# Performance work log

Hardware: AMD Instinct MI355X
Metric: run time of the kernel (lower is better)

## Reference

```python
import jax, jax.numpy as jnp
import numpy as np


def _gauss_kernel(scale):
    # se3cnn.util low_pass_filter: sigma = 0.5*sqrt(scale^2-1), size ~ 1+2*2.5*sigma (odd)
    sigma = 0.5 * float(np.sqrt(scale ** 2 - 1))
    size = int(1 + 2 * 2.5 * sigma)
    if size % 2 == 0:
        size += 1
    r = np.arange(size, dtype=np.float64) - size // 2
    g = np.exp(-r ** 2 / (2 * sigma ** 2))
    k3 = g[:, None, None] * g[None, :, None] * g[None, None, :]
    return (k3 / k3.sum()).astype(np.float32)

_K2 = jnp.asarray(_gauss_kernel(2))  # 5x5x5 Gaussian, scale=2
_DN = ('NCDHW', 'OIDHW', 'NCDHW')


def low_pass(x, stride):
    # depthwise Gaussian blur, padding = size//2 (=2)
    C = x.shape[1]
    k = jnp.tile(_K2[None, None], (C, 1, 1, 1, 1))  # [C,1,5,5,5]
    return jax.lax.conv_general_dilated(x, k, (stride,) * 3, [(2, 2)] * 3,
                                         dimension_numbers=_DN, feature_group_count=C)


def conv3d(x, w, pad):
    return jax.lax.conv_general_dilated(x, w, (1, 1, 1), [(pad, pad)] * 3,
                                         dimension_numbers=_DN)


def gated(x, n_scalar, caps):
    # caps: list of (multiplicity, 2l+1) for l>=1 capsules
    n_gate = sum(m for m, _ in caps)
    scal = jax.nn.relu(x[:, :n_scalar])
    if n_gate == 0:
        return scal
    gates = jax.nn.sigmoid(x[:, n_scalar:n_scalar + n_gate])
    parts = [scal]
    off = n_scalar + n_gate
    goff = 0
    B = x.shape[0]
    S = x.shape[2:]
    for m, d in caps:
        feat = x[:, off:off + m * d].reshape((B, m, d) + S)
        g = gates[:, goff:goff + m].reshape((B, m, 1) + S)
        parts.append((feat * g).reshape((B, m * d) + S))
        off += m * d
        goff += m
    return jnp.concatenate(parts, axis=1)


def gated_block(x, w, stride, n_scalar, caps):
    # smooth_stride: conv at stride 1, then strided low-pass (scale = stride)
    y = conv3d(x, w, pad=4)
    if stride > 1:
        y = low_pass(y, stride)
    return gated(y, n_scalar, caps)


def setup_inputs() -> dict:
    key = jax.random.key(0)
    ks = jax.random.split(key, 7)

    def w(k, shape):
        fan_in = int(np.prod(shape[1:]))
        return jax.random.normal(k, shape, jnp.float32) / np.sqrt(fan_in)

    return {
        'x': jax.random.normal(ks[0], (16, 1, 32, 32, 32), jnp.float32),
        'W1': w(ks[1], (30, 1, 5, 5, 5)),
        'W2': w(ks[2], (88, 25, 5, 5, 5)),
        'W3': w(ks[3], (96, 72, 5, 5, 5)),
        'W4': w(ks[4], (64, 80, 5, 5, 5)),
        'Wl': jax.random.normal(ks[5], (10, 64), jnp.float32) / 8.0,
        'bl': jnp.zeros((10,), jnp.float32),
    }


def reference(x, W1, W2, W3, W4, Wl, bl):
    h = low_pass(x, 1)                                   # input low-pass, scale=2
    h = gated_block(h, W1, 1, 2, [(2, 3), (2, 5), (1, 7)])   # -> 25 ch, 36^3
    h = gated_block(h, W2, 2, 8, [(8, 3), (8, 5)])           # -> 72 ch, 20^3
    h = gated_block(h, W3, 2, 16, [(8, 3), (8, 5)])          # -> 80 ch, 12^3
    h = gated_block(h, W4, 1, 64, [])                        # -> 64 ch, 16^3
    h = h.reshape(h.shape[0], h.shape[1], -1).mean(-1)       # AvgSpacial -> [B,64]
    # Dropout(p=0.2) is identity at eval time
    return h @ Wl.T + bl                                     # [B,10]
```

## Files before the change

### kernel.cpp

```cpp
#include <hip/hip_runtime.h>
#include <math.h>


struct GaussW { float g[5]; };
#define B_ 16

typedef __attribute__((ext_vector_type(8))) short bh8;
typedef __attribute__((ext_vector_type(16))) float f32v16;
union U128 { uint4 u; bh8 h; };

__device__ inline ushort f2bf(float f) {
  uint u = __float_as_uint(f);
  return (ushort)((u + 0x7FFFu + ((u >> 16) & 1u)) >> 16);
}
__device__ inline uint packbf(float v) {
  ushort hi = f2bf(v);
  float hif = __uint_as_float((uint)hi << 16);
  ushort lo = f2bf(v - hif);
  return ((uint)hi << 16) | lo;
}

template<int NBC, int DZ, int DY, int DX, int AXIS, int EXP>
__global__ __launch_bounds__(256) void blur1d(
    const float* __restrict__ in, float* __restrict__ out, GaussW gw)
{
  constexpr int DZO = DZ + ((AXIS == 2 && EXP) ? 4 : 0);
  constexpr int DYO = DY + ((AXIS == 1 && EXP) ? 4 : 0);
  constexpr int OFF = EXP ? 4 : 2;
  constexpr int NV  = DX / 4;
  constexpr int TOT = NBC * DZO * DYO * NV;
  int idx = blockIdx.x * 256 + threadIdx.x;
  if (idx >= TOT) return;
  int xv = idx % NV;
  int t  = idx / NV;
  int y  = t % DYO;
  t /= DYO;
  int z  = t % DZO;
  int bc = t / DZO;
  const float* p = in + (size_t)bc * DZ * DY * DX;
  float4 s = make_float4(0.f, 0.f, 0.f, 0.f);
  #pragma unroll
  for (int k = 0; k < 5; ++k) {
    int c = (AXIS == 2 ? z : y) + k - OFF;
    if (c < 0 || c >= (AXIS == 2 ? DZ : DY)) continue;
    const float4 v = *(const float4*)(p +
        (AXIS == 2 ? ((size_t)c * DY + y) : ((size_t)z * DY + c)) * DX + 4 * xv);
    float g = gw.g[k];
    s.x = fmaf(g, v.x, s.x);
    s.y = fmaf(g, v.y, s.y);
    s.z = fmaf(g, v.z, s.z);
    s.w = fmaf(g, v.w, s.w);
  }
  *(float4*)(out + (((size_t)bc * DZO + z) * DYO + y) * DX + 4 * xv) = s;
}

template<int NBC, int DZ, int DY, int DXI>
__global__ __launch_bounds__(256) void blur1dx_cvt(
    const float* __restrict__ in, uint* __restrict__ out, GaussW gw)
{
  constexpr int DXO = DXI + 4;
  static_assert(DXO % 4 == 0, "DXO must be /4");
  constexpr int NV  = DXO / 4;
  constexpr int TOT = NBC * DZ * DY * NV;
  int idx = blockIdx.x * 256 + threadIdx.x;
  if (idx >= TOT) return;
  int xv = idx % NV;
  int t  = idx / NV;
  int y  = t % DY;
  t /= DY;
  int z  = t % DZ;
  int bc = t / DZ;
  const float* row = in + ((size_t)bc * DZ + z) * DY * DXI + (size_t)y * DXI;
  float win[12];
  #pragma unroll
  for (int q = 0; q < 12; ++q) {
    int gx = 4 * xv + q - 4;
    win[q] = (gx >= 0 && gx < DXI) ? row[gx] : 0.f;
  }
  uint4 po;
  uint* pp = (uint*)&po;
  #pragma unroll
  for (int q = 0; q < 4; ++q) {
    float s = 0.f;
    #pragma unroll
    for (int k = 0; k < 5; ++k) s = fmaf(gw.g[k], win[q + k], s);
    pp[q] = packbf(s);
  }
  *(uint4*)(out + (((size_t)bc * DZ + z) * DY + y) * DXO + 4 * xv) = po;
}

template<int CIN, int COUT, int COP>
__global__ __launch_bounds__(256) void k_transpose_w(
    const float* __restrict__ W, float* __restrict__ Wt)
{
  constexpr int TOT = CIN * 125 * COP;
  int idx = blockIdx.x * 256 + threadIdx.x;
  if (idx >= TOT) return;
  int co = idx % COP;
  int k  = (idx / COP) % 125;
  int ci = idx / (COP * 125);
  Wt[idx] = (co < COUT) ? W[((size_t)co * CIN + ci) * 125 + k] : 0.f;
}

template<int CIN, int NCHUNK, int COUT, int NCOT>
__global__ __launch_bounds__(256) void k_prep_w(
    const float* __restrict__ W, ushort* __restrict__ wf)
{
  constexpr int TOT = NCHUNK * 125 * NCOT * 2 * 512;
  int idx = blockIdx.x * 256 + threadIdx.x;
  if (idx >= TOT) return;
  int j    = idx & 7;
  int lane = (idx >> 3) & 63;
  int hl   = (idx >> 9) & 1;
  int t2   = idx >> 10;
  int cot  = t2 % NCOT;
  int kst  = t2 / NCOT;
  int tap  = kst % 125;
  int chunk = kst / 125;
  int ci = chunk * 16 + (lane >> 5) * 8 + j;
  int co = cot * 32 + (lane & 31);
  float w = 0.f;
  if (ci < CIN && co < COUT) w = W[((size_t)co * CIN + ci) * 125 + tap];
  ushort hi = f2bf(w);
  ushort v = hi;
  if (hl) { float hif = __uint_as_float((uint)hi << 16); v = f2bf(w - hif); }
  wf[idx] = v;
}

template<int S, int CIN, int NCHUNK, int COUT, int NCOT, int DIN, int DOUT,
         int PAD>
__global__ __launch_bounds__(NCOT * 64)
void convM(const uint* __restrict__ in, const ushort* __restrict__ wf,
           float* __restrict__ out)
{
  constexpr int ZT = 2, YT = 4, XT = 4;
  constexpr int ZIN = (ZT - 1) * S + 5;
  constexpr int YIN = (YT - 1) * S + 5;
  constexpr int XIN = (XT - 1) * S + 5;
  constexpr int NPTS = ZIN * YIN * XIN;
  constexpr int RUS = 36;
  constexpr int NTH = NCOT * 64;
  constexpr int NXT = DOUT / XT, NYT = DOUT / YT, NZT = DOUT / ZT;
  static_assert(DOUT % XT == 0 && DOUT % YT == 0 && DOUT % ZT == 0, "tiles");
  constexpr int D2 = DOUT * DOUT;

  __shared__ __align__(16) uint s_in[NPTS * (RUS / 2)];
  ushort* s_us = (ushort*)s_in;

  const int tid  = threadIdx.x;
  const int lane = tid & 63;
  const int cot  = tid >> 6;
  int bxi = blockIdx.x;
  const int xt = bxi % NXT; bxi /= NXT;
  const int yt = bxi % NYT; bxi /= NYT;
  const int zt = bxi % NZT;
  const int b  = bxi / NZT;
  const int z0 = zt * ZT, y0 = yt * YT, x0 = xt * XT;

  const int n  = lane & 31, g = lane >> 5;
  const int zp = n >> 4, ny = (n >> 2) & 3, nx = n & 3;
  const int zl0 = S * zp, yl0 = S * ny, xl0 = S * nx;

  f32v16 ahh, ahl, alh;
  #pragma unroll
  for (int i = 0; i < 16; ++i) { ahh[i] = 0.f; ahl[i] = 0.f; alh[i] = 0.f; }

  #pragma unroll 1
  for (int chunk = 0; chunk < NCHUNK; ++chunk) {
    __syncthreads();
    #pragma unroll 1
    for (int e = tid; e < 16 * NPTS; e += NTH) {
      int cil = e / NPTS;
      int pt  = e - cil * NPTS;
      int sz = pt / (YIN * XIN);
      int r2 = pt - sz * (YIN * XIN);
      int sy = r2 / XIN;
      int sx = r2 - sy * XIN;
      int ci = chunk * 16 + cil;
      int gz = z0 * S + sz - PAD;
      int gy = y0 * S + sy - PAD;
      int gx = x0 * S + sx - PAD;
      uint pk = 0;
      if (ci < CIN && gz >= 0 && gz < DIN && gy >= 0 && gy < DIN &&
          gx >= 0 && gx < DIN)
        pk = in[((size_t)b * CIN + ci) * (DIN * DIN * DIN) +
                (size_t)gz * (DIN * DIN) + gy * DIN + gx];
      s_us[pt * RUS + cil]      = (ushort)(pk >> 16);
      s_us[pt * RUS + 16 + cil] = (ushort)(pk & 0xFFFFu);
    }
    __syncthreads();
    const ushort* wfc = wf + (size_t)chunk * 125 * NCOT * 2 * 512;
    #pragma unroll 1
    for (int kz = 0; kz < 5; ++kz) {
      #pragma unroll 1
      for (int ky = 0; ky < 5; ++ky) {
        const int rowb = ((zl0 + kz) * YIN + (yl0 + ky)) * XIN + xl0;
        for (int kx = 0; kx < 5; ++kx) {
          int tap = (kz * 5 + ky) * 5 + kx;
          const uint4* ap =
              (const uint4*)(wfc + (size_t)((tap * NCOT + cot) * 2) * 512);
          U128 wa, wl;
          wa.u = ap[lane];
          wl.u = ap[64 + lane];
          int pt = rowb + kx;
          const uint2* hp = (const uint2*)(s_us + pt * RUS + 8 * g);
          uint2 h0 = hp[0], h1 = hp[1];
          const uint2* lp = (const uint2*)(s_us + pt * RUS + 16 + 8 * g);
          uint2 l0 = lp[0], l1 = lp[1];
          U128 bh, bl;
          bh.u = make_uint4(h0.x, h0.y, h1.x, h1.y);
          bl.u = make_uint4(l0.x, l0.y, l1.x, l1.y);
          ahh = __builtin_amdgcn_mfma_f32_32x32x16_bf16(wa.h, bh.h, ahh, 0, 0, 0);
          ahl = __builtin_amdgcn_mfma_f32_32x32x16_bf16(wa.h, bl.h, ahl, 0, 0, 0);
          alh = __builtin_amdgcn_mfma_f32_32x32x16_bf16(wl.h, bh.h, alh, 0, 0, 0);
        }
      }
    }
  }
  #pragma unroll
  for (int r = 0; r < 16; ++r) {
    int co = cot * 32 + (r & 3) + 8 * (r >> 2) + 4 * g;
    if (co < COUT) {
      float s = ahh[r] + ahl[r] + alh[r];
      out[(((size_t)b * COUT + co) * DOUT + (z0 + zp)) * D2 +
          (size_t)(y0 + ny) * DOUT + (x0 + nx)] = s;
    }
  }
}

template<int S, int CIN, int CSPLIT, int COUT, int COP, int COB, int NCB,
         int DIN, int XSRC, int DOUT, int PAD, int ZT, int YT, int XB,
         int SPTP, int FUSEX, int XOFF, int CIB>
__global__ __launch_bounds__(256)
void convK(const float* __restrict__ in, const float* __restrict__ wt,
           float* __restrict__ out, size_t split_stride, GaussW gw)
{
  constexpr int K = 5;
  static_assert(DOUT % XB == 0, "XB must divide DOUT");
  constexpr int XQ  = DOUT / XB;
  constexpr int SPT = ZT * YT * XQ;
  static_assert(SPT <= SPTP, "SPTP too small");
  constexpr int NTH = SPTP * NCB;
  static_assert(NTH == 256, "block size 256");
  constexpr int XIN = (DOUT - 1) * S + K;
  constexpr int YIN = (YT - 1) * S + K;
  constexpr int ZIN = (ZT - 1) * S + K;
  constexpr int HXP = (S == 2) ? ((DOUT + 2 + 3) & ~3) : 0;
  constexpr int RW0 = (S == 2) ? (2 * HXP) : ((XIN + 3) & ~3);
  constexpr int RW  = (RW0 % 32 == 0 || RW0 % 32 == 16) ? (RW0 + 4) : RW0;
  constexpr int NROW = ZIN * YIN;
  constexpr int NIN  = NROW * RW;
  static_assert(DOUT % ZT == 0, "ZT must divide DOUT");
  constexpr int NZT = DOUT / ZT;
  constexpr int NYT = (DOUT + YT - 1) / YT;
  constexpr int D2  = DOUT * DOUT;
  constexpr int CI_PER = CIN / CSPLIT;
  static_assert(CI_PER % CIB == 0, "CIB must divide CI_PER");

  __shared__ __align__(16) float s_in[CIB][NIN];

  const int tid = threadIdx.x;
  const int cbg = __builtin_amdgcn_readfirstlane(tid / SPTP);
  const int sp  = tid % SPTP;

  const int bxi = blockIdx.x;
  const int yt  = bxi % NYT;
  const int zt  = (bxi / NYT) % NZT;
  const int b   = bxi / (NYT * NZT);
  const int cb  = blockIdx.y;
  const int spl = blockIdx.z;
  const int co0 = cb * (COB * NCB) + cbg * COB;
  const int oz0 = zt * ZT;
  const int oy0 = yt * YT;
  const int ci0 = spl * CI_PER;

  bool act = sp < SPT;
  int txq = act ? sp % XQ : 0;
  int t2  = act ? sp / XQ : 0;
  int tyl = t2 % YT;
  int tzl = t2 / YT;
  act = act && (oy0 + tyl < DOUT);
  if (!act) { txq = 0; tyl = 0; tzl = 0; }

  float acc[XB][COB];
  #pragma unroll
  for (int j = 0; j < XB; ++j)
    #pragma unroll
    for (int c = 0; c < COB; ++c) acc[j][c] = 0.f;

  for (int r = 0; r < CI_PER; r += CIB) {
    __syncthreads();
    for (int i = tid; i < CIB * NIN; i += NTH) {
      int cc = i / NIN;
      int w  = i - cc * NIN;
      int row = w / RW;
      int wx  = w - row * RW;
      int sz = row / YIN;
      int sy = row - sz * YIN;
      int u;
      if (S == 2) u = (wx < HXP) ? (2 * wx) : (wx < 2 * HXP ? 2 * (wx - HXP) + 1 : -1);
      else        u = (wx < XIN) ? wx : -1;
      int gz = oz0 * S + sz - PAD;
      int gy = oy0 * S + sy - PAD;
      int gx = u - PAD;
      float v = 0.f;
      if (u >= 0 && gz >= 0 && gz < DIN && gy >= 0 && gy < DIN &&
          gx >= 0 && gx < DIN) {
        const float* src = in +
            (((size_t)b * CIN + (ci0 + r + cc)) * DIN + gz) * ((size_t)DIN * XSRC) +
            (size_t)gy * XSRC;
        if constexpr (FUSEX) {
          float sacc = 0.f;
          #pragma unroll
          for (int tp = 0; tp < 5; ++tp) {
            int xs = gx + tp - XOFF;
            if (xs >= 0 && xs < XSRC) sacc = fmaf(gw.g[tp], src[xs], sacc);
          }
          v = sacc;
        } else {
          v = src[gx];
        }
      }
      s_in[cc][w] = v;
    }
    __syncthreads();
    #pragma unroll 1
    for (int cc = 0; cc < CIB; ++cc) {
      const int ci = ci0 + r + cc;
      const float* wci = wt + (size_t)ci * 125 * COP + co0;
      #pragma unroll 1
      for (int kz = 0; kz < K; ++kz) {
        #pragma unroll 1
        for (int ky = 0; ky < K; ++ky) {
          const float* rp = &s_in[cc][((tzl * S + kz) * YIN + (tyl * S + ky)) * RW];
          float fe[8], fo[8];
          if constexpr (S == 2) {
            const float* ep = rp + XB * txq;
            const float* op = rp + HXP + XB * txq;
            #pragma unroll
            for (int q = 0; q < 4; ++q) {
              float2 a = *(const float2*)(ep + 2 * q);
              fe[2*q] = a.x; fe[2*q+1] = a.y;
              float2 b2 = *(const float2*)(op + 2 * q);
              fo[2*q] = b2.x; fo[2*q+1] = b2.y;
            }
          } else {
            const float* wp0 = rp + XB * txq;
            float4 a = *(const float4*)wp0, b4 = *(const float4*)(wp0 + 4);
            fe[0]=a.x; fe[1]=a.y; fe[2]=a.z; fe[3]=a.w;
            fe[4]=b4.x; fe[5]=b4.y; fe[6]=b4.z; fe[7]=b4.w;
            fo[0]=0.f; fo[1]=0.f; fo[2]=0.f; fo[3]=0.f;
            fo[4]=0.f; fo[5]=0.f; fo[6]=0.f; fo[7]=0.f;
          }
          const float* wk = wci + (kz * 25 + ky * 5) * COP;
          #pragma unroll
          for (int kx = 0; kx < K; ++kx) {
            const float* wp = wk + kx * COP;
            float wv[COB];
            #pragma unroll
            for (int c = 0; c < COB; ++c) wv[c] = wp[c];
            #pragma unroll
            for (int j = 0; j < XB; ++j) {
              float iv;
              if constexpr (S == 2)
                iv = (kx & 1) ? fo[j + (kx >> 1)] : fe[j + (kx >> 1)];
              else
                iv = fe[j + kx];
              #pragma unroll
              for (int c = 0; c < COB; ++c)
                acc[j][c] = fmaf(iv, wv[c], acc[j][c]);
            }
          }
        }
      }
    }
  }
  if (act) {
    const int oz = oz0 + tzl, oy = oy0 + tyl, ox = txq * XB;
    float* ob = out + (size_t)spl * split_stride;
    #pragma unroll
    for (int c = 0; c < COB; ++c) {
      int co = co0 + c;
      if (co < COUT) {
        float* p = ob + (((size_t)b * COUT + co) * DOUT + oz) * D2 +
                   (size_t)oy * DOUT + ox;
        #pragma unroll
        for (int q = 0; q < XB / 2; ++q)
          *(float2*)(p + 2 * q) = make_float2(acc[2*q][c], acc[2*q+1][c]);
      }
    }
  }
}

__global__ __launch_bounds__(256) void k_gated4(
    const float* __restrict__ in, float* __restrict__ out,
    int S3v, int Cin, int n_scalar, int n_gate,
    int m1, int d1, int m2, int d2, int m3, int d3, int n_out)
{
  int idx = blockIdx.x * 256 + threadIdx.x;
  int oc = blockIdx.y;
  int b  = blockIdx.z;
  if (idx >= S3v) return;
  size_t S3 = (size_t)S3v * 4;
  auto ld = [&](int ch) {
    return *(const float4*)(in + ((size_t)b * Cin + ch) * S3 + 4 * (size_t)idx);
  };
  float4 val;
  if (oc < n_scalar) {
    float4 v = ld(oc);
    val = make_float4(fmaxf(v.x, 0.f), fmaxf(v.y, 0.f),
                      fmaxf(v.z, 0.f), fmaxf(v.w, 0.f));
  } else {
    int o = oc - n_scalar;
    int gate_ch;
    if (o < m1 * d1) gate_ch = n_scalar + o / d1;
    else if (o - m1 * d1 < m2 * d2) gate_ch = n_scalar + m1 + (o - m1 * d1) / d2;
    else gate_ch = n_scalar + m1 + m2 + (o - m1 * d1 - m2 * d2) / d3;
    float4 v = ld(n_scalar + n_gate + o);
    float4 g = ld(gate_ch);
    val = make_float4(v.x / (1.f + expf(-g.x)), v.y / (1.f + expf(-g.y)),
                      v.z / (1.f + expf(-g.z)), v.w / (1.f + expf(-g.w)));
  }
  *(float4*)(out + ((size_t)b * n_out + oc) * S3 + 4 * (size_t)idx) = val;
}

__global__ __launch_bounds__(256) void k_gated_pack(
    const float* __restrict__ in, uint* __restrict__ out,
    int S3v, int Cin, int n_scalar, int n_gate,
    int m1, int d1, int m2, int d2, int n_out)
{
  int idx = blockIdx.x * 256 + threadIdx.x;
  int oc = blockIdx.y;
  int b  = blockIdx.z;
  if (idx >= S3v) return;
  size_t S3 = (size_t)S3v * 4;
  auto ld = [&](int ch) {
    return *(const float4*)(in + ((size_t)b * Cin + ch) * S3 + 4 * (size_t)idx);
  };
  float4 val;
  if (oc < n_scalar) {
    float4 v = ld(oc);
    val = make_float4(fmaxf(v.x, 0.f), fmaxf(v.y, 0.f),
                      fmaxf(v.z, 0.f), fmaxf(v.w, 0.f));
  } else {
    int o = oc - n_scalar;
    int gate_ch;
    if (o < m1 * d1) gate_ch = n_scalar + o / d1;
    else gate_ch = n_scalar + m1 + (o - m1 * d1) / d2;
    float4 v = ld(n_scalar + n_gate + o);
    float4 g = ld(gate_ch);
    val = make_float4(v.x / (1.f + expf(-g.x)), v.y / (1.f + expf(-g.y)),
                      v.z / (1.f + expf(-g.z)), v.w / (1.f + expf(-g.w)));
  }
  uint4 po = make_uint4(packbf(val.x), packbf(val.y), packbf(val.z),
                        packbf(val.w));
  *(uint4*)(out + ((size_t)b * n_out + oc) * S3 + 4 * (size_t)idx) = po;
}

__global__ __launch_bounds__(256) void k_relu_avg(
    const float* __restrict__ in, float* __restrict__ h)
{
  int bc = blockIdx.x;
  const float* p = in + (size_t)bc * 4096;
  float s = 0.f;
  for (int i = threadIdx.x; i < 1024; i += 256) {
    float4 v = *(const float4*)(p + 4 * i);
    s += fmaxf(v.x, 0.f) + fmaxf(v.y, 0.f) + fmaxf(v.z, 0.f) + fmaxf(v.w, 0.f);
  }
  #pragma unroll
  for (int off = 32; off > 0; off >>= 1) s += __shfl_down(s, off, 64);
  __shared__ float wsum[4];
  int wid = threadIdx.x >> 6;
  if ((threadIdx.x & 63) == 0) wsum[wid] = s;
  __syncthreads();
  if (threadIdx.x == 0)
    h[bc] = (wsum[0] + wsum[1] + wsum[2] + wsum[3]) * (1.f / 4096.f);
}

__global__ __launch_bounds__(256) void k_linear(
    const float* __restrict__ h, const float* __restrict__ Wl,
    const float* __restrict__ bl, float* __restrict__ out)
{
  int t = threadIdx.x;
  if (t >= 160) return;
  int b = t / 10, o = t - b * 10;
  const float* hp = h + b * 64;
  const float* wp = Wl + o * 64;
  float s = bl[o];
  #pragma unroll
  for (int c = 0; c < 64; ++c) s = fmaf(hp[c], wp[c], s);
  out[t] = s;
}

extern "C" void kernel_launch(void* const* d_in, const int* in_sizes, int n_in,
                              void* d_out, int out_size, void* d_ws, size_t ws_size,
                              hipStream_t stream)
{
  const float* x  = (const float*)d_in[0];
  const float* W1 = (const float*)d_in[1];
  const float* W2 = (const float*)d_in[2];
  const float* W3 = (const float*)d_in[3];
  const float* W4 = (const float*)d_in[4];
  const float* Wl = (const float*)d_in[5];
  const float* bl = (const float*)d_in[6];
  float* out = (float*)d_out;
  float* ws  = (float*)d_ws;

  GaussW gw;
  {
    double gv[5], sum = 0.0;
    for (int i = 0; i < 5; ++i) { double r = i - 2; gv[i] = exp(-r * r / 1.5); sum += gv[i]; }
    for (int i = 0; i < 5; ++i) gw.g[i] = (float)(gv[i] / sum);
  }

  size_t off = 0;
  auto A = [&](size_t n) { size_t o = off; off += (n + 63) & ~(size_t)63; return o; };
  size_t o_lp  = A(524288);
  size_t o_W1t = A(4000);
  size_t o_Wf2 = A(384000);
  size_t o_Wf3 = A(960000);
  size_t o_Wf4 = A(640000);
  size_t o_h   = A(1024);
  size_t o_A   = A(23040000);
  size_t o_B   = A(25600000);
  if (ws_size < off * sizeof(float)) return;

  float*  lp  = ws + o_lp;
  float*  W1t = ws + o_W1t;
  ushort* Wf2 = (ushort*)(ws + o_Wf2);
  ushort* Wf3 = (ushort*)(ws + o_Wf3);
  ushort* Wf4 = (ushort*)(ws + o_Wf4);
  float*  hb  = ws + o_h;
  float*  Ab  = ws + o_A;
  float*  Bb  = ws + o_B;

  k_transpose_w<1, 30, 32><<<16, 256, 0, stream>>>(W1, W1t);
  k_prep_w<25, 2, 88, 3><<<(768000 + 255) / 256, 256, 0, stream>>>(W2, Wf2);
  k_prep_w<72, 5, 96, 3><<<(1920000 + 255) / 256, 256, 0, stream>>>(W3, Wf3);
  k_prep_w<80, 5, 64, 2><<<(1280000 + 255) / 256, 256, 0, stream>>>(W4, Wf4);

  blur1d<16, 32, 32, 32, 2, 0><<<(16 * 32 * 32 * 8 + 255) / 256, 256, 0, stream>>>(x, Ab, gw);
  blur1d<16, 32, 32, 32, 1, 0><<<(16 * 32 * 32 * 8 + 255) / 256, 256, 0, stream>>>(Ab, lp, gw);

  convK<1, 1, 1, 30, 32, 8, 2, 32, 32, 36, 4, 2, 7, 4, 128, 1, 2, 1>
      <<<dim3(16 * 18 * 6, 2, 1), 256, 0, stream>>>(lp, W1t, Bb, 0, gw);
  k_gated4<<<dim3(46, 25, 16), 256, 0, stream>>>(Bb, Ab, 11664, 30, 2, 5,
                                                 2, 3, 2, 5, 1, 7, 25);
  blur1d<400, 36, 36, 36, 2, 1><<<(400 * 40 * 36 * 9 + 255) / 256, 256, 0, stream>>>(Ab, Bb, gw);
  blur1d<400, 40, 36, 36, 1, 1><<<(400 * 40 * 40 * 9 + 255) / 256, 256, 0, stream>>>(Bb, Ab, gw);
  blur1dx_cvt<400, 40, 40, 36><<<(400 * 40 * 40 * 10 + 255) / 256, 256, 0, stream>>>(
      Ab, (uint*)Bb, gw);
  convM<2, 25, 2, 88, 3, 40, 20, 2>
      <<<dim3(16 * 10 * 5 * 5), 192, 0, stream>>>((const uint*)Bb, Wf2, Ab);
  k_gated4<<<dim3(8, 72, 16), 256, 0, stream>>>(Ab, Bb, 2000, 88, 8, 16,
                                                8, 3, 8, 5, 0, 1, 72);
  blur1d<1152, 20, 20, 20, 2, 1><<<(1152 * 24 * 20 * 5 + 255) / 256, 256, 0, stream>>>(Bb, Ab, gw);
  blur1d<1152, 24, 20, 20, 1, 1><<<(1152 * 24 * 24 * 5 + 255) / 256, 256, 0, stream>>>(Ab, Bb, gw);
  blur1dx_cvt<1152, 24, 24, 20><<<(1152 * 24 * 24 * 6 + 255) / 256, 256, 0, stream>>>(
      Bb, (uint*)Ab, gw);
  convM<2, 72, 5, 96, 3, 24, 12, 2>
      <<<dim3(16 * 6 * 3 * 3), 192, 0, stream>>>((const uint*)Ab, Wf3, Bb);
  k_gated_pack<<<dim3(2, 80, 16), 256, 0, stream>>>(Bb, (uint*)Ab, 432, 96,
                                                    16, 16, 8, 3, 8, 5, 80);
  convM<1, 80, 5, 64, 2, 12, 16, 4>
      <<<dim3(16 * 8 * 4 * 4), 128, 0, stream>>>((const uint*)Ab, Wf4, Bb);
  k_relu_avg<<<1024, 256, 0, stream>>>(Bb, hb);
  k_linear<<<1, 256, 0, stream>>>(hb, Wl, bl, out);
}
```

Baseline: 2.337 ms.

## Split convM staging into hi/lo passes with row-wise loads and smaller LDS

convM now stages the input tile in two passes per channel chunk. The first pass holds only the high bf16 halves and feeds the hh and lh MFMAs; the second reloads the tile as low halves and feeds the hl MFMA. The fill loop walks whole x-rows per thread with an unrolled inner loop instead of decoding every element, and the LDS row stride drops from 36 to 20 ushorts. This roughly halves LDS use, which may raise occupancy, and makes the index math cheaper. In exchange, global input reads and barriers per chunk double, and the weight tile is fetched again in the second pass.

```diff
diff --git a/kernel.cpp b/kernel.cpp
--- a/kernel.cpp
+++ b/kernel.cpp
@@ -138,14 +138,14 @@
   constexpr int YIN = (YT - 1) * S + 5;
   constexpr int XIN = (XT - 1) * S + 5;
   constexpr int NPTS = ZIN * YIN * XIN;
-  constexpr int RUS = 36;
+  constexpr int RUSP = 20;
   constexpr int NTH = NCOT * 64;
   constexpr int NXT = DOUT / XT, NYT = DOUT / YT, NZT = DOUT / ZT;
   static_assert(DOUT % XT == 0 && DOUT % YT == 0 && DOUT % ZT == 0, "tiles");
   constexpr int D2 = DOUT * DOUT;
-
-  __shared__ __align__(16) uint s_in[NPTS * (RUS / 2)];
-  ushort* s_us = (ushort*)s_in;
+  constexpr int NROWT = 16 * ZIN * YIN;
+
+  __shared__ __align__(16) ushort s_b[NPTS * RUSP];
 
   const int tid  = threadIdx.x;
   const int lane = tid & 63;
@@ -167,52 +167,62 @@
 
   #pragma unroll 1
   for (int chunk = 0; chunk < NCHUNK; ++chunk) {
-    __syncthreads();
-    #pragma unroll 1
-    for (int e = tid; e < 16 * NPTS; e += NTH) {
-      int cil = e / NPTS;
-      int pt  = e - cil * NPTS;
-      int sz = pt / (YIN * XIN);
-      int r2 = pt - sz * (YIN * XIN);
-      int sy = r2 / XIN;
-      int sx = r2 - sy * XIN;
-      int ci = chunk * 16 + cil;
-      int gz = z0 * S + sz - PAD;
-      int gy = y0 * S + sy - PAD;
-      int gx = x0 * S + sx - PAD;
-      uint pk = 0;
-      if (ci < CIN && gz >= 0 && gz < DIN && gy >= 0 && gy < DIN &&
-          gx >= 0 && gx < DIN)
-        pk = in[((size_t)b * CIN + ci) * (DIN * DIN * DIN) +
-                (size_t)gz * (DIN * DIN) + gy * DIN + gx];
-      s_us[pt * RUS + cil]      = (ushort)(pk >> 16);
-      s_us[pt * RUS + 16 + cil] = (ushort)(pk & 0xFFFFu);
-    }
-    __syncthreads();
     const ushort* wfc = wf + (size_t)chunk * 125 * NCOT * 2 * 512;
-    #pragma unroll 1
-    for (int kz = 0; kz < 5; ++kz) {
+    #pragma unroll
+    for (int p = 0; p < 2; ++p) {
+      __syncthreads();
       #pragma unroll 1
-      for (int ky = 0; ky < 5; ++ky) {
-        const int rowb = ((zl0 + kz) * YIN + (yl0 + ky)) * XIN + xl0;
-        for (int kx = 0; kx < 5; ++kx) {
-          int tap = (kz * 5 + ky) * 5 + kx;
-          const uint4* ap =
-              (const uint4*)(wfc + (size_t)((tap * NCOT + cot) * 2) * 512);
-          U128 wa, wl;
-          wa.u = ap[lane];
-          wl.u = ap[64 + lane];
-          int pt = rowb + kx;
-          const uint2* hp = (const uint2*)(s_us + pt * RUS + 8 * g);
-          uint2 h0 = hp[0], h1 = hp[1];
-          const uint2* lp = (const uint2*)(s_us + pt * RUS + 16 + 8 * g);
-          uint2 l0 = lp[0], l1 = lp[1];
-          U128 bh, bl;
-          bh.u = make_uint4(h0.x, h0.y, h1.x, h1.y);
-          bl.u = make_uint4(l0.x, l0.y, l1.x, l1.y);
-          ahh = __builtin_amdgcn_mfma_f32_32x32x16_bf16(wa.h, bh.h, ahh, 0, 0, 0);
-          ahl = __builtin_amdgcn_mfma_f32_32x32x16_bf16(wa.h, bl.h, ahl, 0, 0, 0);
-          alh = __builtin_amdgcn_mfma_f32_32x32x16_bf16(wl.h, bh.h, alh, 0, 0, 0);
+      for (int task = tid; task < NROWT; task += NTH) {
+        int cil = task / (ZIN * YIN);
+        int r   = task - cil * (ZIN * YIN);
+        int sz  = r / YIN;
+        int sy  = r - sz * YIN;
+        int ci = chunk * 16 + cil;
+        int gz = z0 * S + sz - PAD;
+        int gy = y0 * S + sy - PAD;
+        bool rv = (ci < CIN) && (gz >= 0) && (gz < DIN) && (gy >= 0) &&
+                  (gy < DIN);
+        const uint* src = in + ((size_t)b * CIN + ci) * (DIN * DIN * DIN) +
+                          (size_t)gz * (DIN * DIN) + (size_t)gy * DIN;
+        int lb = ((sz * YIN + sy) * XIN) * RUSP + cil;
+        #pragma unroll
+        for (int sx = 0; sx < XIN; ++sx) {
+          int gx = x0 * S + sx - PAD;
+          uint pk = 0;
+          if (rv && gx >= 0 && gx < DIN) pk = src[gx];
+          s_b[lb + sx * RUSP] = (p == 0) ? (ushort)(pk >> 16) : (ushort)pk;
+        }
+      }
+      __syncthreads();
+      #pragma unroll 1
+      for (int kz = 0; kz < 5; ++kz) {
+        #pragma unroll 1
+        for (int ky = 0; ky < 5; ++ky) {
+          const int rowb = ((zl0 + kz) * YIN + (yl0 + ky)) * XIN + xl0;
+          #pragma unroll
+          for (int kx = 0; kx < 5; ++kx) {
+            int tap = (kz * 5 + ky) * 5 + kx;
+            const uint4* ap =
+                (const uint4*)(wfc + (size_t)((tap * NCOT + cot) * 2) * 512);
+            int pt = rowb + kx;
+            const uint2* bp = (const uint2*)(s_b + pt * RUSP + 8 * g);
+            uint2 b0 = bp[0], b1 = bp[1];
+            U128 bb;
+            bb.u = make_uint4(b0.x, b0.y, b1.x, b1.y);
+            U128 wa;
+            wa.u = ap[lane];
+            if (p == 0) {
+              U128 wl;
+              wl.u = ap[64 + lane];
+              ahh = __builtin_amdgcn_mfma_f32_32x32x16_bf16(wa.h, bb.h, ahh,
+                                                            0, 0, 0);
+              alh = __builtin_amdgcn_mfma_f32_32x32x16_bf16(wl.h, bb.h, alh,
+                                                            0, 0, 0);
+            } else {
+              ahl = __builtin_amdgcn_mfma_f32_32x32x16_bf16(wa.h, bb.h, ahl,
+                                                            0, 0, 0);
+            }
+          }
         }
       }
     }
```

Result: faster. 2.201 ms (-5.8%).
